# Optimization experiments

Hardware: AMD Instinct MI355X
Metric: run time of the kernel (lower is better)

Reference implementation:

```python
import jax, jax.numpy as jnp
import numpy as np

# HyenaConfig constants (match init_kwargs)
SEQ_LEN = 8192
HIDDEN_DIM = 768
EMB_DIM = 3
FILTER_ORDER = 64
FAST_DECAY_PCT = 0.3
SLOW_DECAY_PCT = 1.5
TARGET = 0.01
SHIFT = 0.0


def setup_inputs() -> dict:
    key = jax.random.key(0)
    ks = jax.random.split(key, 9)
    return {
        "x": jax.random.normal(ks[0], (8, SEQ_LEN, HIDDEN_DIM), dtype=jnp.float32),
        "w_in": jax.random.normal(ks[1], (EMB_DIM, FILTER_ORDER), dtype=jnp.float32),
        "b_in": jax.random.normal(ks[2], (FILTER_ORDER,), dtype=jnp.float32),
        "freq_in": jnp.ones((1, FILTER_ORDER), dtype=jnp.float32),
        "w_h0": jax.random.normal(ks[3], (FILTER_ORDER, FILTER_ORDER), dtype=jnp.float32),
        "b_h0": jax.random.normal(ks[4], (FILTER_ORDER,), dtype=jnp.float32),
        "freq_h0": jnp.ones((1, FILTER_ORDER), dtype=jnp.float32),
        "w_h1": jax.random.normal(ks[5], (FILTER_ORDER, FILTER_ORDER), dtype=jnp.float32),
        "b_h1": jax.random.normal(ks[6], (FILTER_ORDER,), dtype=jnp.float32),
        "freq_h1": jnp.ones((1, FILTER_ORDER), dtype=jnp.float32),
        "w_out": jax.random.normal(ks[7], (FILTER_ORDER, HIDDEN_DIM), dtype=jnp.float32),
        "bias": jax.random.normal(ks[8], (HIDDEN_DIM,), dtype=jnp.float32),
        "L": SEQ_LEN,
    }


def _pos_emb(L):
    # PositionalEmbedding.init: t in [0,1], z = [t, Re(e^{-i f w}), Im(e^{-i f w})]
    t = jnp.linspace(0.0, 1.0, L, dtype=jnp.float32).reshape(L, 1)
    bands = (EMB_DIM - 1) // 2
    t_rescaled = jnp.linspace(0.0, L - 1, L, dtype=jnp.float32).reshape(L, 1)
    w = 2.0 * jnp.pi * t_rescaled / L  # (L, 1)
    f = jnp.linspace(1e-4, bands - 1, bands, dtype=jnp.float32).reshape(1, bands)
    phase = f * w  # (L, bands)
    z = jnp.concatenate([t, jnp.cos(phase), -jnp.sin(phase)], axis=-1)  # (L, EMB_DIM)
    return z, t


def _filter_k(L, w_in, b_in, freq_in, w_h0, b_h0, freq_h0, w_h1, b_h1, freq_h1, w_out):
    z, t = _pos_emb(L)
    # ImplicitFilterMLP: Linear -> Sin -> (Linear -> Sin) x2 -> Linear (no bias)
    h = jnp.sin(freq_in * (z @ w_in + b_in))
    h = jnp.sin(freq_h0 * (h @ w_h0 + b_h0))
    h = jnp.sin(freq_h1 * (h @ w_h1 + b_h1))
    h = h @ w_out  # (L, HIDDEN_DIM)
    # ExponentialModulation
    max_decay = jnp.log(TARGET) / FAST_DECAY_PCT
    min_decay = jnp.log(TARGET) / SLOW_DECAY_PCT
    deltas = jnp.linspace(min_decay, max_decay, HIDDEN_DIM, dtype=jnp.float32)  # (D,)
    decay = jnp.exp(-t * jnp.abs(deltas))  # (L, D)
    return h * (decay + SHIFT)


def _fft_conv(u, k, bias):
    # u: (B, L, D), k: (L, D)
    seqlen = u.shape[-2]
    fft_size = 2 * seqlen
    u_f = jnp.fft.rfft(u, n=fft_size, axis=-2)
    k_f = jnp.fft.rfft(k[None], n=fft_size, axis=-2) / fft_size
    y = jnp.fft.irfft(u_f * k_f, n=fft_size, axis=-2)[..., :seqlen, :]
    return y + bias.reshape(1, 1, -1)


def reference(x, w_in, b_in, freq_in, w_h0, b_h0, freq_h0, w_h1, b_h1, freq_h1,
              w_out, bias, L):
    k = _filter_k(L, w_in, b_in, freq_in, w_h0, b_h0, freq_h0, w_h1, b_h1,
                  freq_h1, w_out)  # (L, D)
    return _fft_conv(x, k, bias)
```

## Files before the change

kernel.cpp:

```cpp
#include <hip/hip_runtime.h>
#include <stdint.h>

typedef __bf16   bf16x8 __attribute__((ext_vector_type(8)));
typedef float    f32x4  __attribute__((ext_vector_type(4)));
typedef uint32_t u32x4  __attribute__((ext_vector_type(4)));
typedef uint32_t u32x2  __attribute__((ext_vector_type(2)));
typedef unsigned short u16x8 __attribute__((ext_vector_type(8)));

#define L_SEQ 8192
#define DIM   768
#define DROW  8768


__global__ __launch_bounds__(256) void pad_kernel(uint32_t* __restrict__ dupG)
{
  int d = blockIdx.x;
  const int NPAD = 31 + (DROW - 8224);
  for (int j = threadIdx.x; j < NPAD; j += 256) {
    int i = (j < 31) ? j : 8224 + (j - 31);
    dupG[(size_t)d * DROW + i] = 0u;
  }
}

__global__ __launch_bounds__(256) void filter_kernel(
    const float* __restrict__ w_in, const float* __restrict__ b_in,
    const float* __restrict__ freq_in,
    const float* __restrict__ w_h0, const float* __restrict__ b_h0,
    const float* __restrict__ freq_h0,
    const float* __restrict__ w_h1, const float* __restrict__ b_h1,
    const float* __restrict__ freq_h1,
    const float* __restrict__ w_out,
    uint32_t* __restrict__ dupG)
{
  __shared__ float h1[33][65];
  __shared__ float h2[33][65];
  __shared__ unsigned short kv[33][64];
  __shared__ float wch[64][64];

  const int c = blockIdx.x;
  const int dcg = blockIdx.y;
  const int sbase = c << 5;
  const int tid = threadIdx.x;

  for (int p = tid; p < 33 * 64; p += 256) {
    int j = p >> 6, n = p & 63;
    int s = sbase - 1 + j;
    float t  = s * (1.0f / 8191.0f);
    float ph = s * (float)(6.283185307179586 * 1e-4 / 8192.0);
    float a = t * w_in[n] + cosf(ph) * w_in[64 + n] + (-sinf(ph)) * w_in[128 + n] + b_in[n];
    h1[j][n] = sinf(freq_in[n] * a);
  }
  for (int p = tid; p < 64 * 64; p += 256) wch[p >> 6][p & 63] = w_h0[p];
  __syncthreads();
  for (int p = tid; p < 33 * 64; p += 256) {
    int j = p >> 6, n = p & 63;
    float a = b_h0[n];
    for (int r = 0; r < 64; ++r) a += h1[j][r] * wch[r][n];
    h2[j][n] = sinf(freq_h0[n] * a);
  }
  __syncthreads();
  for (int p = tid; p < 64 * 64; p += 256) wch[p >> 6][p & 63] = w_h1[p];
  __syncthreads();
  for (int p = tid; p < 33 * 64; p += 256) {
    int j = p >> 6, n = p & 63;
    float a = b_h1[n];
    for (int r = 0; r < 64; ++r) a += h2[j][r] * wch[r][n];
    h1[j][n] = sinf(freq_h1[n] * a);
  }
  __syncthreads();

  for (int dc = dcg * 3; dc < dcg * 3 + 3; ++dc) {
    for (int p = tid; p < 64 * 64; p += 256) {
      int r = p >> 6, dd = p & 63;
      wch[r][dd] = w_out[r * DIM + dc * 64 + dd];
    }
    __syncthreads();
    for (int p = tid; p < 33 * 64; p += 256) {
      int j = p >> 6, dd = p & 63;
      float a = 0.0f;
      for (int r = 0; r < 64; ++r) a += h1[j][r] * wch[r][dd];
      int s = sbase - 1 + j;
      int d = dc * 64 + dd;
      float delta = fabsf(-3.070113457f - 12.280453827f * (d * (1.0f / 767.0f)));
      float t = s * (1.0f / 8191.0f);
      float val = (s < 0) ? 0.0f : a * expf(-t * delta) * 6.103515625e-05f;
      kv[j][dd] = __builtin_bit_cast(unsigned short, (__bf16)val);
    }
    __syncthreads();
    for (int p = tid; p < 32 * 64; p += 256) {
      int j = p >> 6, dd = p & 63;
      int d = dc * 64 + dd;
      int i = 8223 - (sbase + j);
      dupG[(size_t)d * DROW + i] =
          (uint32_t)kv[j + 1][dd] | ((uint32_t)kv[j][dd] << 16);
    }
    if (c == 255 && tid < 64) {
      int d = dc * 64 + tid;
      dupG[(size_t)d * DROW + 31] = ((uint32_t)kv[32][tid] << 16);
    }
    __syncthreads();
  }
}

__global__ __launch_bounds__(256) void transpose_in_kernel(
    const float* __restrict__ x, unsigned short* __restrict__ uT)
{
  __shared__ unsigned short tile[64][68];
  int b = blockIdx.z;
  int t0 = blockIdx.y * 64;
  int d0 = blockIdx.x * 64;
  int tid = threadIdx.x;

  int ld = tid & 15;
  int tq = tid >> 4;
#pragma unroll
  for (int it = 0; it < 4; ++it) {
    int trow = tq + 16 * it;
    f32x4 xv = *(const f32x4*)&x[((size_t)b * L_SEQ + t0 + trow) * DIM + d0 + 4 * ld];
    unsigned short s0 = __builtin_bit_cast(unsigned short, (__bf16)xv[0]);
    unsigned short s1 = __builtin_bit_cast(unsigned short, (__bf16)xv[1]);
    unsigned short s2 = __builtin_bit_cast(unsigned short, (__bf16)xv[2]);
    unsigned short s3 = __builtin_bit_cast(unsigned short, (__bf16)xv[3]);
    u32x2 pk = { (uint32_t)s0 | ((uint32_t)s1 << 16),
                 (uint32_t)s2 | ((uint32_t)s3 << 16) };
    *(u32x2*)&tile[trow][4 * ld] = pk;
  }
  __syncthreads();

  int l = tid & 63, w = tid >> 6;
  int toct = l & 7;
#pragma unroll
  for (int it = 0; it < 2; ++it) {
    int d = 8 * w + 32 * it + (l >> 3);
    u16x8 o;
#pragma unroll
    for (int c2 = 0; c2 < 8; ++c2) o[c2] = tile[8 * toct + c2][d];
    *(u16x8*)&uT[((size_t)(d0 + d) * 8 + b) * L_SEQ + t0 + 8 * toct] = o;
  }
}

#define LOADFRAG(dst, absdw) {                                    \
    int _p = ((absdw) & 2047);                                    \
    u32x4 _u = { buf[_p], buf[_p + 2], buf[_p + 4], buf[_p + 6] };\
    dst = __builtin_bit_cast(bf16x8, _u); }

#define DSREAD_A(rr, P) (*(const bf16x8*)((P) + abyte + ((rr) << 6)))

typedef __attribute__((address_space(1))) const void g_void;
typedef __attribute__((address_space(3))) void lds_void;

__global__ __launch_bounds__(256) void conv_kernel(
    const uint32_t* __restrict__ dupG,
    const unsigned short* __restrict__ uT,
    unsigned short* __restrict__ yT)
{
  const int d   = blockIdx.y;
  const int T0  = blockIdx.x << 10;
  const int tid = threadIdx.x;
  const int lane = tid & 63;
  const int w    = tid >> 6;
  const int m = lane & 15, q = lane >> 4;
  const int h = (lane >> 3) & 1;
  __shared__ uint32_t buf[2080];
  __shared__ __align__(16) char As0[5120];
  __shared__ __align__(16) char As1[5120];

  f32x4 acc[8] = {};
  bf16x8 fr2[8];
  bf16x8 zfr = {};

  float delta = fabsf(-3.070113457f - 12.280453827f * (d * (1.0f / 767.0f)));
  int S = (int)(8191.0f * 3.5065578f / delta);
  int tau_start = T0 - S;
  tau_start = (tau_start < 0) ? 0 : (tau_start & ~31);
  int niter = ((T0 + 992 - tau_start) >> 5) + 1;
  niter = (niter + 7) & ~7;

  const uint32_t* dG = dupG + (size_t)d * DROW;
  const unsigned short* uTd = uT + ((size_t)d << 16);

  int i0 = 7200 + tau_start - T0;

  int s0 = tid;
  int b0 = s0 / 34, r0 = s0 - 34 * b0;
  const char* ga0 = (const char*)uTd + b0 * 16384 + (tau_start - 16 + r0 * 8) * 2;
  int s1 = 256 + lane;
  int b1 = s1 / 34, r1 = s1 - 34 * b1;
  const char* ga1 = (const char*)uTd + b1 * 16384 + (tau_start - 16 + r1 * 8) * 2;

  const char* Acur = As0;
  const char* Anxt = As1;

  __builtin_amdgcn_global_load_lds((g_void*)ga0, (lds_void*)(As0 + (w << 10)), 16, 0, 0);
  if (w == 0)
    __builtin_amdgcn_global_load_lds((g_void*)ga1, (lds_void*)(As0 + 4096), 16, 0, 0);
  ga0 += 512; ga1 += 512;

  for (int j4 = tid * 4; j4 < 1280; j4 += 1024) {
    int i = i0 + j4;
    u32x4 v = *(const u32x4*)&dG[i];
    int pos = i & 2047;
    *(u32x4*)&buf[pos] = v;
    if (pos < 32) *(u32x4*)&buf[2048 + pos] = v;
  }
  __syncthreads();

  const int abyte = 544 * (lane & 7) + (h << 5) + (q << 4);

  int vb = i0 + 1007 - (w << 8) - m + (q << 3);
  int chunk_i = i0 + 1280;

  LOADFRAG(fr2[7], vb - 32);
  LOADFRAG(fr2[6], vb - 64);
  LOADFRAG(fr2[5], vb - 96);
  LOADFRAG(fr2[4], vb - 128);
  LOADFRAG(fr2[3], vb - 160);
  LOADFRAG(fr2[2], vb - 192);
  LOADFRAG(fr2[1], vb - 224);

  bf16x8 pa_c = DSREAD_A(0, Acur);
  if ((tau_start == 0) & (h == 0) & (q < 2)) pa_c = zfr;

#define MFMA_J(rr, j)                                                          \
  acc[j] = __builtin_amdgcn_mfma_f32_16x16x32_bf16(                            \
      afrag, fr2[((rr) - (j)) & 7], acc[j], 0, 0, 0);

#define BODYP(rr) {                                                            \
    LOADFRAG(fr2[(rr) & 7], vb + ((rr) << 5));                                 \
    bf16x8 afrag = pa_c;                                                       \
    pa_c = DSREAD_A((rr) + 1, Acur);                                           \
    MFMA_J(rr, 1) MFMA_J(rr, 2) MFMA_J(rr, 3) MFMA_J(rr, 4)                    \
    MFMA_J(rr, 5) MFMA_J(rr, 6) MFMA_J(rr, 7) MFMA_J(rr, 0)                    \
  }
#define BODYL(rr) {                                                            \
    LOADFRAG(fr2[(rr) & 7], vb + ((rr) << 5));                                 \
    bf16x8 afrag = pa_c;                                                       \
    MFMA_J(rr, 1) MFMA_J(rr, 2) MFMA_J(rr, 3) MFMA_J(rr, 4)                    \
    MFMA_J(rr, 5) MFMA_J(rr, 6) MFMA_J(rr, 7) MFMA_J(rr, 0)                    \
  }

  for (int nn = 0; nn < niter; nn += 8) {
    __builtin_amdgcn_global_load_lds((g_void*)ga0, (lds_void*)(Anxt + (w << 10)), 16, 0, 0);
    if (w == 0)
      __builtin_amdgcn_global_load_lds((g_void*)ga1, (lds_void*)(Anxt + 4096), 16, 0, 0);
    ga0 += 512; ga1 += 512;
    u32x4 stage = {};
    int si4 = chunk_i + (tid << 2);
    if (tid < 64) {
      int iv = (si4 < 8740) ? si4 : 8740;
      stage = *(const u32x4*)&dG[iv];
    }
    BODYP(0) BODYP(1) BODYP(2) BODYP(3)
    BODYP(4) BODYP(5) BODYP(6) BODYL(7)
    if (tid < 64) {
      int pos = si4 & 2047;
      *(u32x4*)&buf[pos] = stage;
      if (pos < 32) *(u32x4*)&buf[2048 + pos] = stage;
    }
    __syncthreads();
    { const char* t_ = Acur; Acur = Anxt; Anxt = t_; }
    vb += 256; chunk_i += 256;
    pa_c = DSREAD_A(0, Acur);
  }

#pragma unroll
  for (int j = 0; j < 8; ++j) {
    int tb_ = T0 + (w << 8) + (j << 5) + m;
#pragma unroll
    for (int r = 0; r < 4; ++r) {
      int row = q * 4 + r;
      int bb = row & 7;
      int hh = row >> 3;
      yT[((size_t)(d * 8 + bb) << 13) + tb_ + (hh << 4)] =
          __builtin_bit_cast(unsigned short, (__bf16)acc[j][r]);
    }
  }
}

__global__ __launch_bounds__(256) void transpose_out_kernel(
    const unsigned short* __restrict__ yT, const float* __restrict__ bias,
    float* __restrict__ out)
{
  __shared__ unsigned short tile[64][68];
  int b = blockIdx.z;
  int t0 = blockIdx.y * 64;
  int d0 = blockIdx.x * 64;
  int tid = threadIdx.x;

  int l = tid & 63, w = tid >> 6;
  int toct = l & 7;
#pragma unroll
  for (int it = 0; it < 2; ++it) {
    int d = 8 * w + 32 * it + (l >> 3);
    u16x8 o = *(const u16x8*)&yT[((size_t)(d0 + d) * 8 + b) * L_SEQ + t0 + 8 * toct];
#pragma unroll
    for (int c2 = 0; c2 < 8; ++c2) tile[8 * toct + c2][d] = o[c2];
  }
  __syncthreads();

  int ld = tid & 15;
  int tq = tid >> 4;
  f32x4 bs = *(const f32x4*)&bias[d0 + 4 * ld];
#pragma unroll
  for (int it = 0; it < 4; ++it) {
    int trow = tq + 16 * it;
    u32x2 pk = *(const u32x2*)&tile[trow][4 * ld];
    f32x4 ov;
    ov[0] = (float)__builtin_bit_cast(__bf16, (unsigned short)(pk[0] & 0xffff)) + bs[0];
    ov[1] = (float)__builtin_bit_cast(__bf16, (unsigned short)(pk[0] >> 16))    + bs[1];
    ov[2] = (float)__builtin_bit_cast(__bf16, (unsigned short)(pk[1] & 0xffff)) + bs[2];
    ov[3] = (float)__builtin_bit_cast(__bf16, (unsigned short)(pk[1] >> 16))    + bs[3];
    *(f32x4*)&out[((size_t)b * L_SEQ + t0 + trow) * DIM + d0 + 4 * ld] = ov;
  }
}

extern "C" void kernel_launch(void* const* d_in, const int* in_sizes, int n_in,
                              void* d_out, int out_size, void* d_ws, size_t ws_size,
                              hipStream_t stream)
{
  const float* x       = (const float*)d_in[0];
  const float* w_in    = (const float*)d_in[1];
  const float* b_in    = (const float*)d_in[2];
  const float* freq_in = (const float*)d_in[3];
  const float* w_h0    = (const float*)d_in[4];
  const float* b_h0    = (const float*)d_in[5];
  const float* freq_h0 = (const float*)d_in[6];
  const float* w_h1    = (const float*)d_in[7];
  const float* b_h1    = (const float*)d_in[8];
  const float* freq_h1 = (const float*)d_in[9];
  const float* w_out   = (const float*)d_in[10];
  const float* bias    = (const float*)d_in[11];

  char* ws = (char*)d_ws;
  uint32_t* dupG = (uint32_t*)(ws);
  unsigned short* uT = (unsigned short*)(ws + 26935296);
  unsigned short* yT = (unsigned short*)(ws + 127598592);
  float* out = (float*)d_out;

  hipLaunchKernelGGL(pad_kernel, dim3(DIM), dim3(256), 0, stream, dupG);
  hipLaunchKernelGGL(filter_kernel, dim3(256, 4), dim3(256), 0, stream,
                     w_in, b_in, freq_in, w_h0, b_h0, freq_h0,
                     w_h1, b_h1, freq_h1, w_out, dupG);
  hipLaunchKernelGGL(transpose_in_kernel, dim3(12, 128, 8), dim3(256), 0, stream, x, uT);
  hipLaunchKernelGGL(conv_kernel, dim3(8, DIM), dim3(256), 0, stream, dupG, uT, yT);
  hipLaunchKernelGGL(transpose_out_kernel, dim3(12, 128, 8), dim3(256), 0, stream,
                     yT, bias, out);
}
```

Measured before the change: 760.8 us.

## Fold padding into filter kernel, vectorize MLP, and pad conv LDS stride

Removes the separate pad_kernel launch by having each filter_kernel block zero a slice of the padding regions in dupG. The filter MLP and output projection loops now compute four outputs per thread with float4 LDS reads and packed bf16 stores. The conv kernel's A-tile LDS layout moves from a 34-segment row stride (544 bytes) to 35 (560 bytes), likely to avoid LDS bank conflicts, with the extra-load index clamped. This saves one launch and some LDS traffic, but the changed layout must stay consistent with the unseen load and read code.

```diff
diff --git a/kernel.cpp b/kernel.cpp
--- a/kernel.cpp
+++ b/kernel.cpp
@@ -11,16 +11,6 @@
 #define DIM   768
 #define DROW  8768
 
-
-__global__ __launch_bounds__(256) void pad_kernel(uint32_t* __restrict__ dupG)
-{
-  int d = blockIdx.x;
-  const int NPAD = 31 + (DROW - 8224);
-  for (int j = threadIdx.x; j < NPAD; j += 256) {
-    int i = (j < 31) ? j : 8224 + (j - 31);
-    dupG[(size_t)d * DROW + i] = 0u;
-  }
-}
 
 __global__ __launch_bounds__(256) void filter_kernel(
     const float* __restrict__ w_in, const float* __restrict__ b_in,
@@ -42,6 +32,18 @@
   const int sbase = c << 5;
   const int tid = threadIdx.x;
 
+  {
+    int glob = (c << 2) | dcg;
+    int base = glob * 432;
+    for (int k = base + tid; k < base + 432; k += 256) {
+      if (k < 768 * 575) {
+        int dd = k / 575, r = k - dd * 575;
+        int i = (r < 31) ? r : 8224 + (r - 31);
+        dupG[(size_t)dd * DROW + i] = 0u;
+      }
+    }
+  }
+
   for (int p = tid; p < 33 * 64; p += 256) {
     int j = p >> 6, n = p & 63;
     int s = sbase - 1 + j;
@@ -52,20 +54,34 @@
   }
   for (int p = tid; p < 64 * 64; p += 256) wch[p >> 6][p & 63] = w_h0[p];
   __syncthreads();
-  for (int p = tid; p < 33 * 64; p += 256) {
-    int j = p >> 6, n = p & 63;
-    float a = b_h0[n];
-    for (int r = 0; r < 64; ++r) a += h1[j][r] * wch[r][n];
-    h2[j][n] = sinf(freq_h0[n] * a);
+  for (int p = tid; p < 528; p += 256) {
+    int j = p >> 4, n4 = (p & 15) << 2;
+    f32x4 a = *(const f32x4*)&b_h0[n4];
+    for (int r = 0; r < 64; ++r) {
+      f32x4 wv = *(const f32x4*)&wch[r][n4];
+      a += h1[j][r] * wv;
+    }
+    f32x4 f = *(const f32x4*)&freq_h0[n4];
+    h2[j][n4 + 0] = sinf(f[0] * a[0]);
+    h2[j][n4 + 1] = sinf(f[1] * a[1]);
+    h2[j][n4 + 2] = sinf(f[2] * a[2]);
+    h2[j][n4 + 3] = sinf(f[3] * a[3]);
   }
   __syncthreads();
   for (int p = tid; p < 64 * 64; p += 256) wch[p >> 6][p & 63] = w_h1[p];
   __syncthreads();
-  for (int p = tid; p < 33 * 64; p += 256) {
-    int j = p >> 6, n = p & 63;
-    float a = b_h1[n];
-    for (int r = 0; r < 64; ++r) a += h2[j][r] * wch[r][n];
-    h1[j][n] = sinf(freq_h1[n] * a);
+  for (int p = tid; p < 528; p += 256) {
+    int j = p >> 4, n4 = (p & 15) << 2;
+    f32x4 a = *(const f32x4*)&b_h1[n4];
+    for (int r = 0; r < 64; ++r) {
+      f32x4 wv = *(const f32x4*)&wch[r][n4];
+      a += h2[j][r] * wv;
+    }
+    f32x4 f = *(const f32x4*)&freq_h1[n4];
+    h1[j][n4 + 0] = sinf(f[0] * a[0]);
+    h1[j][n4 + 1] = sinf(f[1] * a[1]);
+    h1[j][n4 + 2] = sinf(f[2] * a[2]);
+    h1[j][n4 + 3] = sinf(f[3] * a[3]);
   }
   __syncthreads();
 
@@ -75,16 +91,26 @@
       wch[r][dd] = w_out[r * DIM + dc * 64 + dd];
     }
     __syncthreads();
-    for (int p = tid; p < 33 * 64; p += 256) {
-      int j = p >> 6, dd = p & 63;
-      float a = 0.0f;
-      for (int r = 0; r < 64; ++r) a += h1[j][r] * wch[r][dd];
+    for (int p = tid; p < 528; p += 256) {
+      int j = p >> 4, d4 = (p & 15) << 2;
+      f32x4 a = {};
+      for (int r = 0; r < 64; ++r) {
+        f32x4 wv = *(const f32x4*)&wch[r][d4];
+        a += h1[j][r] * wv;
+      }
       int s = sbase - 1 + j;
-      int d = dc * 64 + dd;
-      float delta = fabsf(-3.070113457f - 12.280453827f * (d * (1.0f / 767.0f)));
       float t = s * (1.0f / 8191.0f);
-      float val = (s < 0) ? 0.0f : a * expf(-t * delta) * 6.103515625e-05f;
-      kv[j][dd] = __builtin_bit_cast(unsigned short, (__bf16)val);
+      unsigned short kq[4];
+#pragma unroll
+      for (int k = 0; k < 4; ++k) {
+        int d = dc * 64 + d4 + k;
+        float delta = fabsf(-3.070113457f - 12.280453827f * (d * (1.0f / 767.0f)));
+        float val = (s < 0) ? 0.0f : a[k] * expf(-t * delta) * 6.103515625e-05f;
+        kq[k] = __builtin_bit_cast(unsigned short, (__bf16)val);
+      }
+      u32x2 pk = { (uint32_t)kq[0] | ((uint32_t)kq[1] << 16),
+                   (uint32_t)kq[2] | ((uint32_t)kq[3] << 16) };
+      *(u32x2*)&kv[j][d4] = pk;
     }
     __syncthreads();
     for (int p = tid; p < 32 * 64; p += 256) {
@@ -182,10 +208,11 @@
   int i0 = 7200 + tau_start - T0;
 
   int s0 = tid;
-  int b0 = s0 / 34, r0 = s0 - 34 * b0;
+  int b0 = s0 / 35, r0 = s0 - 35 * b0;
   const char* ga0 = (const char*)uTd + b0 * 16384 + (tau_start - 16 + r0 * 8) * 2;
   int s1 = 256 + lane;
-  int b1 = s1 / 34, r1 = s1 - 34 * b1;
+  if (s1 > 279) s1 = 279;
+  int b1 = s1 / 35, r1 = s1 - 35 * b1;
   const char* ga1 = (const char*)uTd + b1 * 16384 + (tau_start - 16 + r1 * 8) * 2;
 
   const char* Acur = As0;
@@ -205,7 +232,7 @@
   }
   __syncthreads();
 
-  const int abyte = 544 * (lane & 7) + (h << 5) + (q << 4);
+  const int abyte = 560 * (lane & 7) + (h << 5) + (q << 4);
 
   int vb = i0 + 1007 - (w << 8) - m + (q << 3);
   int chunk_i = i0 + 1280;
@@ -337,7 +364,6 @@
   unsigned short* yT = (unsigned short*)(ws + 127598592);
   float* out = (float*)d_out;
 
-  hipLaunchKernelGGL(pad_kernel, dim3(DIM), dim3(256), 0, stream, dupG);
   hipLaunchKernelGGL(filter_kernel, dim3(256, 4), dim3(256), 0, stream,
                      w_in, b_in, freq_in, w_h0, b_h0, freq_h0,
                      w_h1, b_h1, freq_h1, w_out, dupG);
```

New measurement: 803.2 us. 5.6% more time.
